# Kernel tuning notes

Hardware: AMD Instinct MI355X
Metric: run time of the kernel (lower is better)

The kernel has to match this reference:

```python
import jax, jax.numpy as jnp
import numpy as np
import math

NUM_HEADS = 16
NUM_KV_HEADS = 4
HEAD_DIM = 128
HIDDEN = 2048
ROPE_BASE = 10000.0


def setup_inputs() -> dict:
    key = jax.random.key(0)
    ks = jax.random.split(key, 6)
    B, S = 1, 4096
    hidden_states = jax.random.normal(ks[0], (B, S, HIDDEN), dtype=jnp.float32)
    attention_mask = jnp.ones((B, S), dtype=jnp.int32)
    position_ids = jnp.broadcast_to(jnp.arange(S, dtype=jnp.int32)[None, :], (B, S))
    sc = 1.0 / math.sqrt(HIDDEN)
    wq = jax.random.normal(ks[1], (HIDDEN, NUM_HEADS * HEAD_DIM), dtype=jnp.float32) * sc
    wk = jax.random.normal(ks[2], (HIDDEN, NUM_KV_HEADS * HEAD_DIM), dtype=jnp.float32) * sc
    wv = jax.random.normal(ks[3], (HIDDEN, NUM_KV_HEADS * HEAD_DIM), dtype=jnp.float32) * sc
    wo = jax.random.normal(ks[4], (NUM_HEADS * HEAD_DIM, HIDDEN), dtype=jnp.float32) * sc
    return {"hidden_states": hidden_states, "attention_mask": attention_mask,
            "position_ids": position_ids, "wq": wq, "wk": wk, "wv": wv, "wo": wo}


def _rotate_half(x):
    x1, x2 = jnp.split(x, 2, axis=-1)
    return jnp.concatenate((-x2, x1), axis=-1)


def _rope_tables(seq_len, dtype):
    inv_freq = 1.0 / (ROPE_BASE ** (jnp.arange(0, HEAD_DIM, 2, dtype=jnp.float32) / HEAD_DIM))
    t = jnp.arange(seq_len, dtype=jnp.float32)
    freqs = jnp.outer(t, inv_freq)                       # [S, hd/2]
    emb = jnp.concatenate((freqs, freqs), axis=-1)       # [S, hd]
    return jnp.cos(emb).astype(dtype), jnp.sin(emb).astype(dtype)


def reference(hidden_states, attention_mask, position_ids, wq, wk, wv, wo):
    B, S, _ = hidden_states.shape
    dtype = hidden_states.dtype
    # projections -> [B, H, S, hd]
    q = (hidden_states @ wq).reshape(B, S, NUM_HEADS, HEAD_DIM).transpose(0, 2, 1, 3)
    k = (hidden_states @ wk).reshape(B, S, NUM_KV_HEADS, HEAD_DIM).transpose(0, 2, 1, 3)
    v = (hidden_states @ wv).reshape(B, S, NUM_KV_HEADS, HEAD_DIM).transpose(0, 2, 1, 3)
    # RoPE
    cos_t, sin_t = _rope_tables(S, dtype)
    cos = cos_t[position_ids][:, None]                   # [B,1,S,hd]
    sin = sin_t[position_ids][:, None]
    q = q * cos + _rotate_half(q) * sin
    k = k * cos + _rotate_half(k) * sin
    # GQA repeat
    n_rep = NUM_HEADS // NUM_KV_HEADS
    k = jnp.repeat(k, n_rep, axis=1)
    v = jnp.repeat(v, n_rep, axis=1)
    # scores + causal mask + padding mask
    scores = jnp.einsum('bhqd,bhkd->bhqk', q, k) / math.sqrt(HEAD_DIM)
    neg = jnp.finfo(scores.dtype).min
    causal = jnp.triu(jnp.full((S, S), neg, dtype=scores.dtype), k=1)
    scores = scores + causal[None, None]
    pad = (1.0 - attention_mask.astype(scores.dtype))[:, None, None, :] * neg
    scores = scores + pad
    attn = jax.nn.softmax(scores.astype(jnp.float32), axis=-1).astype(dtype)
    out = jnp.einsum('bhqk,bhkd->bhqd', attn, v)
    out = out.transpose(0, 2, 1, 3).reshape(B, S, NUM_HEADS * HEAD_DIM)
    return out @ wo
```

## Files before the change

kernel.cpp:

```cpp
#include <hip/hip_runtime.h>
#include <cstdint>
#include <cstddef>

typedef unsigned short ushort_t;
typedef short    bf16x8 __attribute__((ext_vector_type(8)));
typedef float    f32x4  __attribute__((ext_vector_type(4)));
typedef uint4    __attribute__((may_alias)) uint4_a;
typedef ushort4  __attribute__((may_alias)) ushort4_a;
typedef float4   __attribute__((may_alias)) float4_a;
typedef unsigned __attribute__((may_alias)) uint_a;

constexpr int SEQ = 4096, HID = 2048, NHEADS = 16, NKVH = 4, HDIM = 128;
constexpr int QD  = NHEADS * HDIM;
constexpr int KVD = NKVH * HDIM;
constexpr int KVL = 2 * KVD;

static __device__ __forceinline__ float bf2f(ushort_t u) {
    return __uint_as_float(((unsigned)u) << 16);
}
static __device__ __forceinline__ ushort_t f2bf(float f) {
    unsigned x = __float_as_uint(f);
    unsigned r = x + 0x7FFFu + ((x >> 16) & 1u);
    return (ushort_t)(r >> 16);
}
static __device__ __forceinline__ unsigned pack2(float lo, float hi) {
    return (unsigned)f2bf(lo) | ((unsigned)f2bf(hi) << 16);
}

static __device__ __forceinline__ void gld16(const ushort_t* g, ushort_t* l) {
    __builtin_amdgcn_global_load_lds(
        (const __attribute__((address_space(1))) unsigned*)g,
        (__attribute__((address_space(3))) unsigned*)l, 16, 0, 0);
}

__global__ __launch_bounds__(256) void cast_f32_bf16(
    const float* __restrict__ in, ushort_t* __restrict__ out, int n)
{
    int i = (blockIdx.x * 256 + threadIdx.x) * 8;
    if (i >= n) return;
    float4 a = *(const float4_a*)(in + i);
    float4 b = *(const float4_a*)(in + i + 4);
    uint4 o;
    o.x = pack2(a.x, a.y); o.y = pack2(a.z, a.w);
    o.z = pack2(b.x, b.y); o.w = pack2(b.z, b.w);
    *(uint4_a*)(out + i) = o;
}

__global__ __launch_bounds__(256) void transpose_cast(
    const float* __restrict__ W, ushort_t* __restrict__ WT, int K, int N)
{
    __shared__ float tl[32][36];
    const int k0 = blockIdx.x * 32, n0 = blockIdx.y * 32;
    const int t  = threadIdx.x;
    {
        int i = t >> 3, jb = (t & 7) * 4;
        *(float4_a*)&tl[i][jb] = *(const float4_a*)(W + (size_t)(k0 + i) * N + n0 + jb);
    }
    __syncthreads();
    {
        int n = t >> 3, kb = (t & 7) * 4;
        ushort4 o;
        o.x = f2bf(tl[kb + 0][n]); o.y = f2bf(tl[kb + 1][n]);
        o.z = f2bf(tl[kb + 2][n]); o.w = f2bf(tl[kb + 3][n]);
        *(ushort4_a*)(WT + (size_t)(n0 + n) * K + k0 + kb) = o;
    }
}

__global__ __launch_bounds__(256) void gemm_mfma(
    const ushort_t* __restrict__ A, int lda,
    const ushort_t* __restrict__ Bt, int ldb,
    void* __restrict__ C1, int ld1, void* __restrict__ C2, int ld2,
    int split, int N, int K, int out_f32)
{
    __shared__ ushort_t as[128 * 32];
    __shared__ ushort_t bs[128 * 32];

    const int t    = threadIdx.x;
    const int mb   = blockIdx.y * 128, nb = blockIdx.x * 128;
    const int w    = t >> 6, lane = t & 63, quad = lane >> 4, l15 = lane & 15;
    const int wm   = (w >> 1) * 64, wn = (w & 1) * 64;

    const int dr_row = lane >> 2, dr_c = lane & 3;
    const int rA0 = w * 16 + dr_row, rA1 = 64 + w * 16 + dr_row;
    const ushort_t* a0p = A  + (size_t)(mb + rA0) * lda + (dr_c ^ (rA0 & 3)) * 8;
    const ushort_t* a1p = A  + (size_t)(mb + rA1) * lda + (dr_c ^ (rA1 & 3)) * 8;
    const ushort_t* b0p = Bt + (size_t)(nb + rA0) * ldb + (dr_c ^ (rA0 & 3)) * 8;
    const ushort_t* b1p = Bt + (size_t)(nb + rA1) * ldb + (dr_c ^ (rA1 & 3)) * 8;
    ushort_t* asb0 = &as[(w) * 512];        ushort_t* asb1 = &as[(4 + w) * 512];
    ushort_t* bsb0 = &bs[(w) * 512];        ushort_t* bsb1 = &bs[(4 + w) * 512];

    f32x4 acc[4][4];
#pragma unroll
    for (int i = 0; i < 4; i++)
#pragma unroll
        for (int j = 0; j < 4; j++) acc[i][j] = (f32x4)0.f;

    const int chunk = quad ^ (l15 & 3);

    for (int kb = 0; kb < K; kb += 32) {
        __syncthreads();
        gld16(a0p + kb, asb0);
        gld16(a1p + kb, asb1);
        gld16(b0p + kb, bsb0);
        gld16(b1p + kb, bsb1);
        __syncthreads();

        bf16x8 af[4], bf[4];
#pragma unroll
        for (int mt = 0; mt < 4; mt++)
            af[mt] = *(const bf16x8*)&as[(wm + mt * 16 + l15) * 32 + chunk * 8];
#pragma unroll
        for (int nt = 0; nt < 4; nt++)
            bf[nt] = *(const bf16x8*)&bs[(wn + nt * 16 + l15) * 32 + chunk * 8];
#pragma unroll
        for (int mt = 0; mt < 4; mt++)
#pragma unroll
            for (int nt = 0; nt < 4; nt++)
                acc[mt][nt] = __builtin_amdgcn_mfma_f32_16x16x32_bf16(
                    af[mt], bf[nt], acc[mt][nt], 0, 0, 0);
    }

#pragma unroll
    for (int mt = 0; mt < 4; mt++)
#pragma unroll
        for (int nt = 0; nt < 4; nt++) {
            int colg = nb + wn + nt * 16 + l15;
#pragma unroll
            for (int r = 0; r < 4; r++) {
                int row = mb + wm + mt * 16 + quad * 4 + r;
                float v = acc[mt][nt][r];
                if (out_f32)            ((float*)C1)[(size_t)row * ld1 + colg] = v;
                else if (colg < split)  ((ushort_t*)C1)[(size_t)row * ld1 + colg] = f2bf(v);
                else                    ((ushort_t*)C2)[(size_t)row * ld2 + colg - split] = f2bf(v);
            }
        }
}

__global__ __launch_bounds__(256) void rope_bf16(
    ushort_t* __restrict__ buf, int ld, int nh, const int* __restrict__ pos_ids)
{
    int idx  = blockIdx.x * 256 + threadIdx.x;
    int i    = idx & 63;
    int rem  = idx >> 6;
    int head = rem % nh;
    int s    = rem / nh;
    if (s >= SEQ) return;

    float pos = (float)pos_ids[s];
    float ang = pos * __expf(-(float)i * 0.14391156831212787f);
    float c, sn;
    sincosf(ang, &sn, &c);

    ushort_t* p = buf + (size_t)s * ld + head * HDIM;
    float x0 = bf2f(p[i]);
    float x1 = bf2f(p[i + 64]);
    p[i]      = f2bf(x0 * c - x1 * sn);
    p[i + 64] = f2bf(x1 * c + x0 * sn);
}

__global__ __launch_bounds__(512, 4) void flash_mfma(
    const ushort_t* Q, const ushort_t* __restrict__ KV,
    const int* __restrict__ amask, ushort_t* O)
{
    __shared__ ushort_t ks[64][136];
    __shared__ ushort_t vt[128][72];
    __shared__ float    bias[64];

    const int t = threadIdx.x, w = t >> 6, lane = t & 63;
    const int quad = lane >> 4, l15 = lane & 15;
    const int h = blockIdx.x, kvh = h >> 2;
    const int q0 = (gridDim.y - 1 - blockIdx.y) * 128;
    const int q0w = q0 + w * 16;
    const int kcol = kvh * HDIM, vcol = KVD + kvh * HDIM;

    bf16x8 qf[4];
    {
        const ushort_t* qp = Q + (size_t)(q0w + l15) * QD + h * HDIM;
#pragma unroll
        for (int c = 0; c < 4; c++)
            qf[c] = *(const bf16x8*)(qp + c * 32 + quad * 8);
    }

    f32x4 accO[8];
#pragma unroll
    for (int j = 0; j < 8; j++) accO[j] = (f32x4)0.f;
    float m_s = -1e30f, l_s = 0.f;
    const float scale2 = 0.08838834764831845f * 1.44269504088896340f;

    const int krow = t >> 3,  kdo = (t & 7) * 16;
    const int vkp  = t & 31,  vdg = t >> 5;

    int bpi[4];
#pragma unroll
    for (int t4 = 0; t4 < 4; t4++)
        bpi[t4] = ((2 * (quad & 1) + (t4 >> 1)) * 16 + l15) * 4;
    const bool hi_half = (quad >> 1) != 0;

    uint4 kst[2], va, vb;
    float bst = 0.f;
    auto stage_load = [&](int kt) {
        const int k0 = kt * 64;
        const ushort_t* kp = KV + (size_t)(k0 + krow) * KVL + kcol + kdo;
        kst[0] = *(const uint4_a*)kp;
        kst[1] = *(const uint4_a*)(kp + 8);
        const ushort_t* vp = KV + (size_t)(k0 + 2 * vkp) * KVL + vcol + vdg * 8;
        va = *(const uint4_a*)vp;
        vb = *(const uint4_a*)(vp + KVL);
        if (t < 64) bst = amask[k0 + t] ? 0.f : -1e30f;
    };

    const int nkt = (q0 >> 6) + 2;
    stage_load(0);

    for (int kt = 0; kt < nkt; kt++) {
        const int k0 = kt * 64;
        __syncthreads();
        *(uint4_a*)&ks[krow][kdo]     = kst[0];
        *(uint4_a*)&ks[krow][kdo + 8] = kst[1];
        {
            unsigned aw[4] = {va.x, va.y, va.z, va.w};
            unsigned bw[4] = {vb.x, vb.y, vb.z, vb.w};
#pragma unroll
            for (int i = 0; i < 4; i++) {
                *(uint_a*)&vt[vdg * 8 + 2 * i][2 * vkp] =
                    (aw[i] & 0xFFFFu) | (bw[i] << 16);
                *(uint_a*)&vt[vdg * 8 + 2 * i + 1][2 * vkp] =
                    (aw[i] >> 16) | (bw[i] & 0xFFFF0000u);
            }
        }
        if (t < 64) bias[t] = bst;
        __syncthreads();
        if (kt + 1 < nkt) stage_load(kt + 1);

        if (k0 > q0w + 15) continue;

        f32x4 s[4];
#pragma unroll
        for (int mt = 0; mt < 4; mt++) s[mt] = (f32x4)0.f;
#pragma unroll
        for (int c = 0; c < 4; c++)
#pragma unroll
            for (int mt = 0; mt < 4; mt++) {
                bf16x8 kf = *(const bf16x8*)&ks[mt * 16 + l15][c * 32 + quad * 8];
                s[mt] = __builtin_amdgcn_mfma_f32_16x16x32_bf16(kf, qf[c], s[mt], 0, 0, 0);
            }

        const int qg = q0w + l15;
        const bool full = (k0 + 63 <= q0w);
        float p[4][4];
        float mx = -1e30f;
#pragma unroll
        for (int mt = 0; mt < 4; mt++) {
            float4 b4 = *(const float4_a*)&bias[mt * 16 + quad * 4];
            float br[4] = {b4.x, b4.y, b4.z, b4.w};
#pragma unroll
            for (int r = 0; r < 4; r++) {
                float v = fmaf(s[mt][r], scale2, br[r]);
                if (!full) {
                    int kg = k0 + mt * 16 + quad * 4 + r;
                    v = (kg > qg) ? -1e30f : v;
                }
                p[mt][r] = v;
                mx = fmaxf(mx, v);
            }
        }
        mx = fmaxf(mx, __shfl_xor(mx, 16));
        mx = fmaxf(mx, __shfl_xor(mx, 32));
        float mnew = fmaxf(m_s, mx);
        float alpha = exp2f(m_s - mnew);
        m_s = mnew;
        float sum = 0.f;
        unsigned wlo[4], whi[4];
#pragma unroll
        for (int mt = 0; mt < 4; mt++) {
            float p0 = exp2f(p[mt][0] - mnew);
            float p1 = exp2f(p[mt][1] - mnew);
            float p2 = exp2f(p[mt][2] - mnew);
            float p3 = exp2f(p[mt][3] - mnew);
            sum += (p0 + p1) + (p2 + p3);
            wlo[mt] = pack2(p0, p1);
            whi[mt] = pack2(p2, p3);
        }
        sum += __shfl_xor(sum, 16);
        sum += __shfl_xor(sum, 32);
        l_s = l_s * alpha + sum;

        {
            float a0 = __shfl(alpha, quad * 4 + 0);
            float a1 = __shfl(alpha, quad * 4 + 1);
            float a2 = __shfl(alpha, quad * 4 + 2);
            float a3 = __shfl(alpha, quad * 4 + 3);
#pragma unroll
            for (int j = 0; j < 8; j++) {
                f32x4 a = accO[j];
                a[0] *= a0; a[1] *= a1; a[2] *= a2; a[3] *= a3;
                accO[j] = a;
            }
        }

#pragma unroll
        for (int kc = 0; kc < 2; kc++) {
            union { unsigned u[4]; bf16x8 v; } pf;
#pragma unroll
            for (int t4 = 0; t4 < 4; t4++) {
                unsigned slo = (t4 & 1) ? whi[2 * kc]     : wlo[2 * kc];
                unsigned shi = (t4 & 1) ? whi[2 * kc + 1] : wlo[2 * kc + 1];
                int ra = __builtin_amdgcn_ds_bpermute(bpi[t4], (int)slo);
                int rb = __builtin_amdgcn_ds_bpermute(bpi[t4], (int)shi);
                pf.u[t4] = (unsigned)(hi_half ? rb : ra);
            }
#pragma unroll
            for (int n8 = 0; n8 < 8; n8++) {
                bf16x8 vf = *(const bf16x8*)&vt[n8 * 16 + l15][kc * 32 + quad * 8];
                accO[n8] = __builtin_amdgcn_mfma_f32_16x16x32_bf16(pf.v, vf, accO[n8], 0, 0, 0);
            }
        }
    }

    float linv = 1.0f / l_s;
#pragma unroll
    for (int r = 0; r < 4; r++) {
        float lr = __shfl(linv, quad * 4 + r);
        int row = q0w + quad * 4 + r;
        ushort_t* op = O + (size_t)row * QD + h * HDIM;
#pragma unroll
        for (int n8 = 0; n8 < 8; n8++)
            op[n8 * 16 + l15] = f2bf(accO[n8][r] * lr);
    }
}

extern "C" void kernel_launch(void* const* d_in, const int* in_sizes, int n_in,
                              void* d_out, int out_size, void* d_ws, size_t ws_size,
                              hipStream_t stream)
{
    const float* x     = (const float*)d_in[0];
    const int*   amask = (const int*)d_in[1];
    const int*   pos   = (const int*)d_in[2];
    const float* wq    = (const float*)d_in[3];
    const float* wk    = (const float*)d_in[4];
    const float* wv    = (const float*)d_in[5];
    const float* wo    = (const float*)d_in[6];
    float* out = (float*)d_out;

    ushort_t* wqkvT = (ushort_t*)d_out;
    ushort_t* xb    = wqkvT + (size_t)3072 * HID;

    ushort_t* qbuf  = (ushort_t*)d_ws;
    ushort_t* kvbuf = qbuf + (size_t)SEQ * QD;
    ushort_t* woT   = kvbuf;

    cast_f32_bf16<<<SEQ * HID / 8 / 256, 256, 0, stream>>>(x, xb, SEQ * HID);
    transpose_cast<<<dim3(HID / 32, QD / 32),  256, 0, stream>>>(wq, wqkvT, HID, QD);
    transpose_cast<<<dim3(HID / 32, KVD / 32), 256, 0, stream>>>(wk, wqkvT + (size_t)QD * HID, HID, KVD);
    transpose_cast<<<dim3(HID / 32, KVD / 32), 256, 0, stream>>>(wv, wqkvT + (size_t)(QD + KVD) * HID, HID, KVD);

    gemm_mfma<<<dim3(3072 / 128, SEQ / 128), 256, 0, stream>>>(
        xb, HID, wqkvT, HID, qbuf, QD, kvbuf, KVL, QD, 3072, HID, 0);

    rope_bf16<<<SEQ * NHEADS * 64 / 256, 256, 0, stream>>>(qbuf, QD, NHEADS, pos);
    rope_bf16<<<SEQ * NKVH  * 64 / 256, 256, 0, stream>>>(kvbuf, KVL, NKVH, pos);

    flash_mfma<<<dim3(NHEADS, SEQ / 128), 512, 0, stream>>>(qbuf, kvbuf, amask, qbuf);

    transpose_cast<<<dim3(QD / 32, HID / 32), 256, 0, stream>>>(wo, woT, QD, HID);
    gemm_mfma<<<dim3(HID / 128, SEQ / 128), 256, 0, stream>>>(
        qbuf, QD, woT, QD, out, HID, out, HID, HID, HID, QD, 1);
}
```

Baseline: 515.3 us.

## Shrink flash attention blocks to 64 queries, add lazy rescale and packed bf16 convert

Flash attention now runs 256-thread blocks covering 64 query rows instead of 512 threads covering 128. Each thread stages twice as much K/V into shared memory, and the block count doubles, which improves causal load balance and occupancy. The online softmax now skips rescaling the accumulators unless the running max grows by more than 8 (log2 units), a lazy-rescale trick. Probabilities are converted with the hardware v_cvt_pk_bf16_f32 instruction instead of software rounding. The trade-off is less K/V reuse per block, plus a small risk to numerical range from the deferred rescale.

```diff
diff --git a/kernel.cpp b/kernel.cpp
--- a/kernel.cpp
+++ b/kernel.cpp
@@ -25,6 +25,11 @@
 }
 static __device__ __forceinline__ unsigned pack2(float lo, float hi) {
     return (unsigned)f2bf(lo) | ((unsigned)f2bf(hi) << 16);
+}
+static __device__ __forceinline__ unsigned cvt_pk(float lo, float hi) {
+    unsigned r;
+    asm("v_cvt_pk_bf16_f32 %0, %1, %2" : "=v"(r) : "v"(lo), "v"(hi));
+    return r;
 }
 
 static __device__ __forceinline__ void gld16(const ushort_t* g, ushort_t* l) {
@@ -158,7 +163,7 @@
     p[i + 64] = f2bf(x1 * c + x0 * sn);
 }
 
-__global__ __launch_bounds__(512, 4) void flash_mfma(
+__global__ __launch_bounds__(256, 4) void flash_mfma(
     const ushort_t* Q, const ushort_t* __restrict__ KV,
     const int* __restrict__ amask, ushort_t* O)
 {
@@ -169,7 +174,7 @@
     const int t = threadIdx.x, w = t >> 6, lane = t & 63;
     const int quad = lane >> 4, l15 = lane & 15;
     const int h = blockIdx.x, kvh = h >> 2;
-    const int q0 = (gridDim.y - 1 - blockIdx.y) * 128;
+    const int q0 = (gridDim.y - 1 - blockIdx.y) * 64;
     const int q0w = q0 + w * 16;
     const int kcol = kvh * HDIM, vcol = KVD + kvh * HDIM;
 
@@ -187,7 +192,7 @@
     float m_s = -1e30f, l_s = 0.f;
     const float scale2 = 0.08838834764831845f * 1.44269504088896340f;
 
-    const int krow = t >> 3,  kdo = (t & 7) * 16;
+    const int krow = t >> 2,  kdo = (t & 3) * 32;
     const int vkp  = t & 31,  vdg = t >> 5;
 
     int bpi[4];
@@ -196,36 +201,51 @@
         bpi[t4] = ((2 * (quad & 1) + (t4 >> 1)) * 16 + l15) * 4;
     const bool hi_half = (quad >> 1) != 0;
 
-    uint4 kst[2], va, vb;
+    uint4 kst0, kst1, kst2, kst3, va0, va1, vb0, vb1;
     float bst = 0.f;
     auto stage_load = [&](int kt) {
         const int k0 = kt * 64;
         const ushort_t* kp = KV + (size_t)(k0 + krow) * KVL + kcol + kdo;
-        kst[0] = *(const uint4_a*)kp;
-        kst[1] = *(const uint4_a*)(kp + 8);
-        const ushort_t* vp = KV + (size_t)(k0 + 2 * vkp) * KVL + vcol + vdg * 8;
-        va = *(const uint4_a*)vp;
-        vb = *(const uint4_a*)(vp + KVL);
+        kst0 = *(const uint4_a*)kp;
+        kst1 = *(const uint4_a*)(kp + 8);
+        kst2 = *(const uint4_a*)(kp + 16);
+        kst3 = *(const uint4_a*)(kp + 24);
+        const ushort_t* vp = KV + (size_t)(k0 + 2 * vkp) * KVL + vcol + vdg * 16;
+        va0 = *(const uint4_a*)vp;
+        va1 = *(const uint4_a*)(vp + 8);
+        vb0 = *(const uint4_a*)(vp + KVL);
+        vb1 = *(const uint4_a*)(vp + KVL + 8);
         if (t < 64) bst = amask[k0 + t] ? 0.f : -1e30f;
     };
 
-    const int nkt = (q0 >> 6) + 2;
+    const int nkt = (q0 >> 6) + 1;
     stage_load(0);
 
     for (int kt = 0; kt < nkt; kt++) {
         const int k0 = kt * 64;
         __syncthreads();
-        *(uint4_a*)&ks[krow][kdo]     = kst[0];
-        *(uint4_a*)&ks[krow][kdo + 8] = kst[1];
+        *(uint4_a*)&ks[krow][kdo]      = kst0;
+        *(uint4_a*)&ks[krow][kdo + 8]  = kst1;
+        *(uint4_a*)&ks[krow][kdo + 16] = kst2;
+        *(uint4_a*)&ks[krow][kdo + 24] = kst3;
         {
-            unsigned aw[4] = {va.x, va.y, va.z, va.w};
-            unsigned bw[4] = {vb.x, vb.y, vb.z, vb.w};
+            unsigned aw[4] = {va0.x, va0.y, va0.z, va0.w};
+            unsigned bw[4] = {vb0.x, vb0.y, vb0.z, vb0.w};
 #pragma unroll
             for (int i = 0; i < 4; i++) {
-                *(uint_a*)&vt[vdg * 8 + 2 * i][2 * vkp] =
+                *(uint_a*)&vt[vdg * 16 + 2 * i][2 * vkp] =
                     (aw[i] & 0xFFFFu) | (bw[i] << 16);
-                *(uint_a*)&vt[vdg * 8 + 2 * i + 1][2 * vkp] =
+                *(uint_a*)&vt[vdg * 16 + 2 * i + 1][2 * vkp] =
                     (aw[i] >> 16) | (bw[i] & 0xFFFF0000u);
+            }
+            unsigned aw2[4] = {va1.x, va1.y, va1.z, va1.w};
+            unsigned bw2[4] = {vb1.x, vb1.y, vb1.z, vb1.w};
+#pragma unroll
+            for (int i = 0; i < 4; i++) {
+                *(uint_a*)&vt[vdg * 16 + 8 + 2 * i][2 * vkp] =
+                    (aw2[i] & 0xFFFFu) | (bw2[i] << 16);
+                *(uint_a*)&vt[vdg * 16 + 8 + 2 * i + 1][2 * vkp] =
+                    (aw2[i] >> 16) | (bw2[i] & 0xFFFF0000u);
             }
         }
         if (t < 64) bias[t] = bst;
@@ -266,9 +286,8 @@
         }
         mx = fmaxf(mx, __shfl_xor(mx, 16));
         mx = fmaxf(mx, __shfl_xor(mx, 32));
-        float mnew = fmaxf(m_s, mx);
-        float alpha = exp2f(m_s - mnew);
-        m_s = mnew;
+        const bool renorm = !__all(mx <= m_s + 8.f);
+        const float mnew = renorm ? fmaxf(m_s, mx) : m_s;
         float sum = 0.f;
         unsigned wlo[4], whi[4];
 #pragma unroll
@@ -278,14 +297,15 @@
             float p2 = exp2f(p[mt][2] - mnew);
             float p3 = exp2f(p[mt][3] - mnew);
             sum += (p0 + p1) + (p2 + p3);
-            wlo[mt] = pack2(p0, p1);
-            whi[mt] = pack2(p2, p3);
+            wlo[mt] = cvt_pk(p0, p1);
+            whi[mt] = cvt_pk(p2, p3);
         }
         sum += __shfl_xor(sum, 16);
         sum += __shfl_xor(sum, 32);
-        l_s = l_s * alpha + sum;
-
-        {
+
+        if (renorm) {
+            float alpha = exp2f(m_s - mnew);
+            l_s *= alpha;
             float a0 = __shfl(alpha, quad * 4 + 0);
             float a1 = __shfl(alpha, quad * 4 + 1);
             float a2 = __shfl(alpha, quad * 4 + 2);
@@ -297,6 +317,8 @@
                 accO[j] = a;
             }
         }
+        m_s = mnew;
+        l_s += sum;
 
 #pragma unroll
         for (int kc = 0; kc < 2; kc++) {
@@ -360,7 +382,7 @@
     rope_bf16<<<SEQ * NHEADS * 64 / 256, 256, 0, stream>>>(qbuf, QD, NHEADS, pos);
     rope_bf16<<<SEQ * NKVH  * 64 / 256, 256, 0, stream>>>(kvbuf, KVL, NKVH, pos);
 
-    flash_mfma<<<dim3(NHEADS, SEQ / 128), 512, 0, stream>>>(qbuf, kvbuf, amask, qbuf);
+    flash_mfma<<<dim3(NHEADS, SEQ / 64), 256, 0, stream>>>(qbuf, kvbuf, amask, qbuf);
 
     transpose_cast<<<dim3(QD / 32, HID / 32), 256, 0, stream>>>(wo, woT, QD, HID);
     gemm_mfma<<<dim3(HID / 128, SEQ / 128), 256, 0, stream>>>(
```

Result: slower. 532.1 us (+3.3%).
